# Performance work log

Measured on AMD Instinct MI355X. Metric: run time of the kernel, lower is better.

The kernel has to match this reference:

```python
import jax, jax.numpy as jnp
import numpy as np

DIM = 256          # channels
HEADS = 8
KS = 3             # kernel_size
DIL = (1, 2, 3, 4) # dilation rates
ND = len(DIL)
HEAD_DIM = DIM // HEADS
SCALE = HEAD_DIM ** -0.5
DPG = DIM // ND    # channels per dilation group
EPS = 1e-5


def setup_inputs() -> dict:
    key = jax.random.key(0)
    ks = jax.random.split(key, 4)
    B, H, W = 8, 64, 64
    vi = jax.random.normal(ks[0], (B, DIM, H, W), jnp.float32)
    ir = jax.random.normal(ks[1], (B, DIM, H, W), jnp.float32)
    w_qkv = jax.random.normal(ks[2], (3 * DIM, DIM), jnp.float32) * 0.02  # 1x1 conv, no bias (qkv_bias=False)
    proj_w = jax.random.normal(ks[3], (DIM, DIM), jnp.float32) * 0.02     # nn.Linear weight
    proj_b = jnp.zeros((DIM,), jnp.float32)
    ln_g = jnp.ones((DIM,), jnp.float32)
    ln_b = jnp.zeros((DIM,), jnp.float32)
    return dict(vi=vi, ir=ir, w_qkv=w_qkv, proj_w=proj_w, proj_b=proj_b, ln_g=ln_g, ln_b=ln_b)


def _unfold(t, dil):
    # t: [B, d, H, W] -> [B, d, KS*KS, H, W], same layout as nn.Unfold(KS, dil, pad=dil*(KS-1)//2)
    B, d, H, W = t.shape
    pad = dil * (KS - 1) // 2
    tp = jnp.pad(t, ((0, 0), (0, 0), (pad, pad), (pad, pad)))
    patches = [tp[:, :, i * dil:i * dil + H, j * dil:j * dil + W]
               for i in range(KS) for j in range(KS)]
    return jnp.stack(patches, axis=2)


def _dilate_attention(q, k, v, dil):
    # q,k,v: [B, d, H, W] with d = DPG; returns [B, H, W, d]
    B, d, H, W = q.shape
    h = d // HEAD_DIM
    N = H * W
    kk = KS * KS
    qf = q.reshape(B, h, HEAD_DIM, N)                      # b h d n
    kf = _unfold(k, dil).reshape(B, h, HEAD_DIM, kk, N)    # b h d k n
    vf = _unfold(v, dil).reshape(B, h, HEAD_DIM, kk, N)
    attn = jax.nn.softmax(jnp.einsum('bhdn,bhdkn->bhnk', qf, kf) * SCALE, axis=-1)
    out = jnp.einsum('bhnk,bhdkn->bhnd', attn, vf)         # b h n d
    return out.transpose(0, 2, 1, 3).reshape(B, H, W, d)   # channel = head*HEAD_DIM + c


def _dilate_block(x, w_qkv, proj_w, proj_b, ln_g, ln_b):
    # x: [B, C, H, W]; DilateBlock: permute -> LN -> MultiDilatelocalAttention -> residual -> permute back
    B, C, H, W = x.shape
    xn = x.transpose(0, 2, 3, 1)                           # B H W C
    mu = jnp.mean(xn, -1, keepdims=True)
    var = jnp.var(xn, -1, keepdims=True)
    xn = (xn - mu) * jax.lax.rsqrt(var + EPS) * ln_g + ln_b
    xc = xn.transpose(0, 3, 1, 2)                          # B C H W
    # 1x1 conv qkv -> [B, 3, ND, DPG, H, W]
    qkv = jnp.einsum('oc,bchw->bohw', w_qkv, xc).reshape(B, 3, ND, DPG, H, W)
    outs = [_dilate_attention(qkv[:, 0, i], qkv[:, 1, i], qkv[:, 2, i], DIL[i])
            for i in range(ND)]                            # each [B, H, W, DPG]
    y = jnp.stack(outs, axis=3).reshape(B, H, W, C)        # channel = dil_idx*DPG + c
    y = y @ proj_w.T + proj_b                              # nn.Linear
    return x + y.transpose(0, 3, 1, 2)                     # residual, back to B C H W


def reference(vi, ir, w_qkv, proj_w, proj_b, ln_g, ln_b):
    sub = vi - ir
    div = _dilate_block(sub, w_qkv, proj_w, proj_b, ln_g, ln_b)
    o = jnp.matmul(vi, div)   # batched [H,W]@[H,W] over (B, C)
    return (o, o)
```

## Files before the change

### kernel.cpp

```cpp
#include <hip/hip_runtime.h>
#include <math.h>

#define B_ 8
#define C_ 256
#define N_ 4096
#define NPOS 32768
#define SCALE_ 0.1767766952966369f
#define EPS_ 1e-5f

typedef __attribute__((ext_vector_type(8))) short bf16x8;
typedef __attribute__((ext_vector_type(8))) unsigned short u16x8;
typedef __attribute__((ext_vector_type(4))) unsigned short u16x4;
typedef __attribute__((ext_vector_type(4))) float f32x4;

__device__ __forceinline__ unsigned short f2bf(float f) {
  union { float f; unsigned u; } v; v.f = f;
  unsigned r = v.u + 0x7fff + ((v.u >> 16) & 1);
  return (unsigned short)(r >> 16);
}
__device__ __forceinline__ float bf2f(unsigned short u) {
  union { unsigned u; float f; } v; v.u = ((unsigned)u) << 16; return v.f;
}
__device__ __forceinline__ float blo(unsigned u) {
  union { unsigned u; float f; } v; v.u = u << 16; return v.f;
}
__device__ __forceinline__ float bhi(unsigned u) {
  union { unsigned u; float f; } v; v.u = u & 0xffff0000u; return v.f;
}

#define GLD_LDS16(g, l) \
  __builtin_amdgcn_global_load_lds((const __attribute__((address_space(1))) unsigned int*)(g), \
                                   (__attribute__((address_space(3))) unsigned int*)(l), 16, 0, 0)

__global__ __launch_bounds__(256) void k_cvt(
    const float* __restrict__ wq, const float* __restrict__ pw,
    unsigned short* __restrict__ dst)
{
  int i4 = blockIdx.x * 256 + threadIdx.x;
  float4 v = (i4 < 49152) ? ((const float4*)wq)[i4] : ((const float4*)pw)[i4 - 49152];
  ushort4 o;
  o.x = f2bf(v.x); o.y = f2bf(v.y); o.z = f2bf(v.z); o.w = f2bf(v.w);
  ((ushort4*)dst)[i4] = o;
}

__global__ __launch_bounds__(256) void k_sub_ln(
    const float* __restrict__ vi, const float* __restrict__ ir,
    const float* __restrict__ ln_g, const float* __restrict__ ln_b,
    unsigned short* __restrict__ subB, unsigned short* __restrict__ xn)
{
  __shared__ float tile[C_ * 33];
  __shared__ float redS[8][32], redS2[8][32];
  __shared__ float meanS[32], rstdS[32];
  int blk = blockIdx.x;
  int b = blk >> 7;
  int y = (blk >> 1) & 63;
  int half = blk & 1;
  int t = threadIdx.x;
  size_t base = (size_t)b * C_ * N_ + (size_t)y * 64 + half * 32;
  #pragma unroll
  for (int it = 0; it < 8; ++it) {
    int c = it * 32 + (t >> 3);
    int xq = (t & 7) * 4;
    size_t g = base + (size_t)c * N_ + xq;
    float4 v4 = *(const float4*)&vi[g];
    float4 i4 = *(const float4*)&ir[g];
    float4 s4;
    s4.x = v4.x - i4.x; s4.y = v4.y - i4.y; s4.z = v4.z - i4.z; s4.w = v4.w - i4.w;
    ushort4 sb;
    sb.x = f2bf(s4.x); sb.y = f2bf(s4.y); sb.z = f2bf(s4.z); sb.w = f2bf(s4.w);
    *(ushort4*)&subB[g] = sb;
    tile[c * 33 + xq + 0] = s4.x;
    tile[c * 33 + xq + 1] = s4.y;
    tile[c * 33 + xq + 2] = s4.z;
    tile[c * 33 + xq + 3] = s4.w;
  }
  __syncthreads();
  {
    int p = t & 31, grp = t >> 5;
    float s = 0.f, s2 = 0.f;
    #pragma unroll
    for (int cc = 0; cc < 32; ++cc) {
      float v = tile[(grp * 32 + cc) * 33 + p];
      s += v; s2 += v * v;
    }
    redS[grp][p] = s; redS2[grp][p] = s2;
  }
  __syncthreads();
  if (t < 32) {
    float s = 0.f, s2 = 0.f;
    #pragma unroll
    for (int g2 = 0; g2 < 8; ++g2) { s += redS[g2][t]; s2 += redS2[g2][t]; }
    float mu = s * (1.f / 256.f);
    float var = s2 * (1.f / 256.f) - mu * mu;
    meanS[t] = mu;
    rstdS[t] = rsqrtf(var + EPS_);
  }
  __syncthreads();
  int c = t;
  float gg = ln_g[c], bb = ln_b[c];
  size_t xbase = ((size_t)b * N_ + (size_t)y * 64 + half * 32) * C_;
  for (int p = 0; p < 32; ++p) {
    float v = (tile[c * 33 + p] - meanS[p]) * rstdS[p] * gg + bb;
    xn[xbase + (size_t)p * C_ + c] = f2bf(v);
  }
}

template<int EPI>
__global__ __launch_bounds__(256) void k_gemm_mfma(
    const unsigned short* __restrict__ A,
    const unsigned short* __restrict__ Bw,
    unsigned short* __restrict__ Cout,
    const float* __restrict__ bias,
    const unsigned short* __restrict__ subB,
    int ldc)
{
  __shared__ __align__(16) unsigned short As[128 * 32];
  __shared__ __align__(16) unsigned short Bs[128 * 32];
  __shared__ __align__(16) unsigned short Cs[64 * 136];
  int tid = threadIdx.x;
  int wv = tid >> 6;
  int lane = tid & 63;
  int m0 = blockIdx.x * 128;
  int n0 = blockIdx.y * 128;
  int mw = (wv >> 1) * 64, nw = (wv & 1) * 64;
  int r = lane & 15, q = lane >> 4;

  int seg0 = wv * 2;
  int srow0 = seg0 * 16 + (lane >> 2);
  int scol = (lane & 3) * 8;
  const unsigned short* ga0 = A  + (size_t)(m0 + srow0) * 256 + scol;
  const unsigned short* ga1 = ga0 + 16 * 256;
  const unsigned short* gb0 = Bw + (size_t)(n0 + srow0) * 256 + scol;
  const unsigned short* gb1 = gb0 + 16 * 256;
  unsigned short* la0 = &As[seg0 * 512];
  unsigned short* la1 = la0 + 512;
  unsigned short* lb0 = &Bs[seg0 * 512];
  unsigned short* lb1 = lb0 + 512;

  f32x4 acc[4][4];
  #pragma unroll
  for (int i = 0; i < 4; ++i)
    #pragma unroll
    for (int j = 0; j < 4; ++j)
      acc[i][j] = (f32x4){0.f, 0.f, 0.f, 0.f};

  for (int k0 = 0; k0 < 256; k0 += 32) {
    GLD_LDS16(ga0 + k0, la0);
    GLD_LDS16(ga1 + k0, la1);
    GLD_LDS16(gb0 + k0, lb0);
    GLD_LDS16(gb1 + k0, lb1);
    __syncthreads();
    bf16x8 af[4], bfr[4];
    #pragma unroll
    for (int mt = 0; mt < 4; ++mt)
      af[mt] = *(const bf16x8*)&As[(mw + mt * 16 + r) * 32 + q * 8];
    #pragma unroll
    for (int nt = 0; nt < 4; ++nt)
      bfr[nt] = *(const bf16x8*)&Bs[(nw + nt * 16 + r) * 32 + q * 8];
    #pragma unroll
    for (int mt = 0; mt < 4; ++mt)
      #pragma unroll
      for (int nt = 0; nt < 4; ++nt)
        acc[mt][nt] = __builtin_amdgcn_mfma_f32_16x16x32_bf16(af[mt], bfr[nt], acc[mt][nt], 0, 0, 0);
    __syncthreads();
  }

  int b = m0 >> 12;
  int nn0 = m0 & 4095;
  #pragma unroll
  for (int pass = 0; pass < 2; ++pass) {
    __syncthreads();
    if (EPI == 0) {
      if ((wv >> 1) == pass) {
        #pragma unroll
        for (int mt = 0; mt < 4; ++mt) {
          int lr = mt * 16 + q * 4;
          #pragma unroll
          for (int nt = 0; nt < 4; ++nt) {
            int col = nw + nt * 16 + r;
            #pragma unroll
            for (int rr = 0; rr < 4; ++rr)
              Cs[(lr + rr) * 136 + col] = f2bf(acc[mt][nt][rr]);
          }
        }
      }
    } else {
      if ((wv & 1) == pass) {
        #pragma unroll
        for (int nt = 0; nt < 4; ++nt) {
          int lr = nt * 16 + r;
          #pragma unroll
          for (int mt = 0; mt < 4; ++mt) {
            int pc = mw + mt * 16 + q * 4;
            #pragma unroll
            for (int rr = 0; rr < 4; ++rr)
              Cs[lr * 136 + pc + rr] = f2bf(acc[mt][nt][rr]);
          }
        }
      }
    }
    __syncthreads();
    if (EPI == 0) {
      #pragma unroll
      for (int cc = 0; cc < 4; ++cc) {
        int ch = cc * 256 + tid;
        int row = ch >> 4, cg = ch & 15;
        u16x8 cv = *(const u16x8*)&Cs[row * 136 + cg * 8];
        int m = m0 + pass * 64 + row;
        *(u16x8*)&Cout[(size_t)m * ldc + n0 + cg * 8] = cv;
      }
    } else {
      #pragma unroll
      for (int cc = 0; cc < 4; ++cc) {
        int ch = cc * 256 + tid;
        int row = ch >> 4, cg = ch & 15;
        u16x8 cv = *(const u16x8*)&Cs[row * 136 + cg * 8];
        int c = n0 + pass * 64 + row;
        size_t idx = ((size_t)(b * 256 + c)) * 4096 + nn0 + cg * 8;
        u16x8 sv = *(const u16x8*)&subB[idx];
        float bb = bias[c];
        u16x8 ov;
        #pragma unroll
        for (int e = 0; e < 8; ++e)
          ov[e] = f2bf(bf2f((unsigned short)cv[e]) + bb + bf2f((unsigned short)sv[e]));
        *(u16x8*)&Cout[idx] = ov;
      }
    }
  }
}

__global__ __launch_bounds__(256) void k_attn(
    const unsigned short* __restrict__ qkv,
    unsigned short* __restrict__ y)
{
  int t = threadIdx.x;
  int sub = t >> 2;
  int lane4 = t & 3;
  int item = blockIdx.x * 64 + sub;
  int ih = item & 7;
  int p = item >> 3;
  int i = ih >> 1, h = ih & 1;
  int dil = i + 1;
  int b = p >> 12;
  int n = p & 4095;
  int py = n >> 6, px = n & 63;
  int off = i * 64 + h * 32 + lane4 * 8;
  const unsigned short* base = qkv + off;

  uint4 qw = *(const uint4*)(base + (size_t)p * 768);
  float q0 = blo(qw.x), q1 = bhi(qw.x), q2 = blo(qw.y), q3 = bhi(qw.y),
        q4 = blo(qw.z), q5 = bhi(qw.z), q6 = blo(qw.w), q7 = bhi(qw.w);

  int pj[9];
  #pragma unroll
  for (int j = 0; j < 9; ++j) {
    int ny = py + (j / 3 - 1) * dil;
    int nx = px + (j % 3 - 1) * dil;
    bool ok = ((unsigned)ny < 64u) && ((unsigned)nx < 64u);
    pj[j] = ok ? ((b << 12) + (ny << 6) + nx) : -1;
  }

  float sc[9];
  #pragma unroll
  for (int j = 0; j < 9; ++j) {
    float s = 0.f;
    if (pj[j] >= 0) {
      uint4 kw = *(const uint4*)(base + 256 + (size_t)pj[j] * 768);
      s  = q0 * blo(kw.x) + q1 * bhi(kw.x);
      s += q2 * blo(kw.y) + q3 * bhi(kw.y);
      s += q4 * blo(kw.z) + q5 * bhi(kw.z);
      s += q6 * blo(kw.w) + q7 * bhi(kw.w);
    }
    s += __shfl_xor(s, 1, 4);
    s += __shfl_xor(s, 2, 4);
    sc[j] = s * SCALE_;
  }

  float mx = sc[0];
  #pragma unroll
  for (int j = 1; j < 9; ++j) mx = fmaxf(mx, sc[j]);
  float e[9], ssum = 0.f;
  #pragma unroll
  for (int j = 0; j < 9; ++j) { e[j] = __expf(sc[j] - mx); ssum += e[j]; }
  float inv = 1.f / ssum;

  float o0 = 0.f, o1 = 0.f, o2 = 0.f, o3 = 0.f, o4 = 0.f, o5 = 0.f, o6 = 0.f, o7 = 0.f;
  #pragma unroll
  for (int j = 0; j < 9; ++j) {
    if (pj[j] >= 0) {
      float w = e[j] * inv;
      uint4 vw = *(const uint4*)(base + 512 + (size_t)pj[j] * 768);
      o0 += w * blo(vw.x); o1 += w * bhi(vw.x);
      o2 += w * blo(vw.y); o3 += w * bhi(vw.y);
      o4 += w * blo(vw.z); o5 += w * bhi(vw.z);
      o6 += w * blo(vw.w); o7 += w * bhi(vw.w);
    }
  }

  u16x8 ov;
  ov[0] = f2bf(o0); ov[1] = f2bf(o1); ov[2] = f2bf(o2); ov[3] = f2bf(o3);
  ov[4] = f2bf(o4); ov[5] = f2bf(o5); ov[6] = f2bf(o6); ov[7] = f2bf(o7);
  *(u16x8*)(y + (size_t)p * 256 + off) = ov;
}

__global__ __launch_bounds__(256) void k_bmm(
    const float* __restrict__ vi, const unsigned short* __restrict__ divmB,
    float* __restrict__ out)
{
  __shared__ float At[64 * 68];
  __shared__ float Bsm[64 * 64];
  int bc = blockIdx.x;
  size_t base = (size_t)bc * 4096;
  int t = threadIdx.x;
  #pragma unroll
  for (int it = 0; it < 4; ++it) {
    int flat = it * 1024 + t * 4;
    int row = flat >> 6, col = flat & 63;
    float4 a = *(const float4*)&vi[base + flat];
    At[(col + 0) * 68 + row] = a.x;
    At[(col + 1) * 68 + row] = a.y;
    At[(col + 2) * 68 + row] = a.z;
    At[(col + 3) * 68 + row] = a.w;
  }
  #pragma unroll
  for (int it = 0; it < 2; ++it) {
    int flat = it * 2048 + t * 8;
    u16x8 dv = *(const u16x8*)&divmB[base + flat];
    float4 lo, hi;
    lo.x = bf2f((unsigned short)dv[0]); lo.y = bf2f((unsigned short)dv[1]);
    lo.z = bf2f((unsigned short)dv[2]); lo.w = bf2f((unsigned short)dv[3]);
    hi.x = bf2f((unsigned short)dv[4]); hi.y = bf2f((unsigned short)dv[5]);
    hi.z = bf2f((unsigned short)dv[6]); hi.w = bf2f((unsigned short)dv[7]);
    *(float4*)&Bsm[flat] = lo;
    *(float4*)&Bsm[flat + 4] = hi;
  }
  __syncthreads();
  int tx = t & 15, ty = t >> 4;
  float acc[4][4] = {};
  for (int k = 0; k < 64; ++k) {
    float4 a = *(const float4*)&At[k * 68 + (ty << 2)];
    float4 b = *(const float4*)&Bsm[k * 64 + (tx << 2)];
    acc[0][0] += a.x * b.x; acc[0][1] += a.x * b.y; acc[0][2] += a.x * b.z; acc[0][3] += a.x * b.w;
    acc[1][0] += a.y * b.x; acc[1][1] += a.y * b.y; acc[1][2] += a.y * b.z; acc[1][3] += a.y * b.w;
    acc[2][0] += a.z * b.x; acc[2][1] += a.z * b.y; acc[2][2] += a.z * b.z; acc[2][3] += a.z * b.w;
    acc[3][0] += a.w * b.x; acc[3][1] += a.w * b.y; acc[3][2] += a.w * b.z; acc[3][3] += a.w * b.w;
  }
  #pragma unroll
  for (int i = 0; i < 4; ++i) {
    int row = (ty << 2) + i;
    float4 w = make_float4(acc[i][0], acc[i][1], acc[i][2], acc[i][3]);
    *(float4*)&out[base + row * 64 + (tx << 2)] = w;
    *(float4*)&out[8388608ull + base + row * 64 + (tx << 2)] = w;
  }
}

extern "C" void kernel_launch(void* const* d_in, const int* in_sizes, int n_in,
                              void* d_out, int out_size, void* d_ws, size_t ws_size,
                              hipStream_t stream) {
  const float* vi     = (const float*)d_in[0];
  const float* ir     = (const float*)d_in[1];
  const float* w_qkv  = (const float*)d_in[2];
  const float* proj_w = (const float*)d_in[3];
  const float* proj_b = (const float*)d_in[4];
  const float* ln_g   = (const float*)d_in[5];
  const float* ln_b   = (const float*)d_in[6];
  float* out = (float*)d_out;
  char* ws = (char*)d_ws;
  unsigned short* subB = (unsigned short*)(ws);
  unsigned short* qkvb = (unsigned short*)(ws + 16777216);
  unsigned short* divmB= (unsigned short*)(ws + 16777216);
  unsigned short* xnb  = (unsigned short*)(ws + 67108864);
  unsigned short* yb   = (unsigned short*)(ws + 83886080);
  unsigned short* wqb  = (unsigned short*)(ws + 100663296);
  unsigned short* pwb  = wqb + 196608;

  k_cvt<<<256, 256, 0, stream>>>(w_qkv, proj_w, wqb);
  k_sub_ln<<<1024, 256, 0, stream>>>(vi, ir, ln_g, ln_b, subB, xnb);
  k_gemm_mfma<0><<<dim3(256, 6), 256, 0, stream>>>(xnb, wqb, qkvb, nullptr, nullptr, 768);
  k_attn<<<4096, 256, 0, stream>>>(qkvb, yb);
  k_gemm_mfma<1><<<dim3(256, 2), 256, 0, stream>>>(yb, pwb, divmB, proj_b, subB, 0);
  k_bmm<<<2048, 256, 0, stream>>>(vi, divmB, out);
}
```

Measured before the change: 215.4 us.

## Use bf16 MFMA for final batched matmul, fuse prep kernels, XCD-aware GEMM tiling

The final per-channel 64x64 matmul moves from fp32 FMA on LDS tiles to bf16 MFMA. It reads a bf16 copy of vi that the fused sub/LayerNorm prep kernel now writes, and the weight-conversion kernel is folded into that same launch. Both GEMMs switch to a 1D grid remapped so that consecutive M-tiles land on the same XCD, which should improve L2 locality. The cost is lower precision in the final matmul, since vi is rounded to bf16, plus an extra 16 MB write of viB and scalar output stores.

```diff
diff --git a/kernel.cpp b/kernel.cpp
--- a/kernel.cpp
+++ b/kernel.cpp
@@ -10,7 +10,6 @@
 
 typedef __attribute__((ext_vector_type(8))) short bf16x8;
 typedef __attribute__((ext_vector_type(8))) unsigned short u16x8;
-typedef __attribute__((ext_vector_type(4))) unsigned short u16x4;
 typedef __attribute__((ext_vector_type(4))) float f32x4;
 
 __device__ __forceinline__ unsigned short f2bf(float f) {
@@ -32,30 +31,30 @@
   __builtin_amdgcn_global_load_lds((const __attribute__((address_space(1))) unsigned int*)(g), \
                                    (__attribute__((address_space(3))) unsigned int*)(l), 16, 0, 0)
 
-__global__ __launch_bounds__(256) void k_cvt(
+__global__ __launch_bounds__(256) void k_pre(
+    const float* __restrict__ vi, const float* __restrict__ ir,
     const float* __restrict__ wq, const float* __restrict__ pw,
-    unsigned short* __restrict__ dst)
-{
-  int i4 = blockIdx.x * 256 + threadIdx.x;
-  float4 v = (i4 < 49152) ? ((const float4*)wq)[i4] : ((const float4*)pw)[i4 - 49152];
-  ushort4 o;
-  o.x = f2bf(v.x); o.y = f2bf(v.y); o.z = f2bf(v.z); o.w = f2bf(v.w);
-  ((ushort4*)dst)[i4] = o;
-}
-
-__global__ __launch_bounds__(256) void k_sub_ln(
-    const float* __restrict__ vi, const float* __restrict__ ir,
     const float* __restrict__ ln_g, const float* __restrict__ ln_b,
-    unsigned short* __restrict__ subB, unsigned short* __restrict__ xn)
+    unsigned short* __restrict__ wdst,
+    unsigned short* __restrict__ subB, unsigned short* __restrict__ viB,
+    unsigned short* __restrict__ xn)
 {
   __shared__ float tile[C_ * 33];
   __shared__ float redS[8][32], redS2[8][32];
   __shared__ float meanS[32], rstdS[32];
-  int blk = blockIdx.x;
+  int t = threadIdx.x;
+  if (blockIdx.x < 256) {
+    int i4 = blockIdx.x * 256 + t;
+    float4 v = (i4 < 49152) ? ((const float4*)wq)[i4] : ((const float4*)pw)[i4 - 49152];
+    ushort4 o;
+    o.x = f2bf(v.x); o.y = f2bf(v.y); o.z = f2bf(v.z); o.w = f2bf(v.w);
+    ((ushort4*)wdst)[i4] = o;
+    return;
+  }
+  int blk = blockIdx.x - 256;
   int b = blk >> 7;
   int y = (blk >> 1) & 63;
   int half = blk & 1;
-  int t = threadIdx.x;
   size_t base = (size_t)b * C_ * N_ + (size_t)y * 64 + half * 32;
   #pragma unroll
   for (int it = 0; it < 8; ++it) {
@@ -66,9 +65,11 @@
     float4 i4 = *(const float4*)&ir[g];
     float4 s4;
     s4.x = v4.x - i4.x; s4.y = v4.y - i4.y; s4.z = v4.z - i4.z; s4.w = v4.w - i4.w;
-    ushort4 sb;
+    ushort4 sb, vb;
     sb.x = f2bf(s4.x); sb.y = f2bf(s4.y); sb.z = f2bf(s4.z); sb.w = f2bf(s4.w);
+    vb.x = f2bf(v4.x); vb.y = f2bf(v4.y); vb.z = f2bf(v4.z); vb.w = f2bf(v4.w);
     *(ushort4*)&subB[g] = sb;
+    *(ushort4*)&viB[g] = vb;
     tile[c * 33 + xq + 0] = s4.x;
     tile[c * 33 + xq + 1] = s4.y;
     tile[c * 33 + xq + 2] = s4.z;
@@ -105,7 +106,7 @@
   }
 }
 
-template<int EPI>
+template<int EPI, int NT>
 __global__ __launch_bounds__(256) void k_gemm_mfma(
     const unsigned short* __restrict__ A,
     const unsigned short* __restrict__ Bw,
@@ -117,11 +118,16 @@
   __shared__ __align__(16) unsigned short As[128 * 32];
   __shared__ __align__(16) unsigned short Bs[128 * 32];
   __shared__ __align__(16) unsigned short Cs[64 * 136];
+  int flat = blockIdx.x;
+  int xcd = flat & 7;
+  int l = flat >> 3;
+  int ml = l / NT;
+  int nn = l - ml * NT;
+  int m0 = (xcd * 32 + ml) * 128;
+  int n0 = nn * 128;
   int tid = threadIdx.x;
   int wv = tid >> 6;
   int lane = tid & 63;
-  int m0 = blockIdx.x * 128;
-  int n0 = blockIdx.y * 128;
   int mw = (wv >> 1) * 64, nw = (wv & 1) * 64;
   int r = lane & 15, q = lane >> 4;
 
@@ -304,54 +310,67 @@
 }
 
 __global__ __launch_bounds__(256) void k_bmm(
-    const float* __restrict__ vi, const unsigned short* __restrict__ divmB,
+    const unsigned short* __restrict__ viB,
+    const unsigned short* __restrict__ divmB,
     float* __restrict__ out)
 {
-  __shared__ float At[64 * 68];
-  __shared__ float Bsm[64 * 64];
+  __shared__ __align__(16) unsigned short Vs[64 * 72];
+  __shared__ __align__(16) unsigned short Ds[64 * 72];
   int bc = blockIdx.x;
   size_t base = (size_t)bc * 4096;
   int t = threadIdx.x;
-  #pragma unroll
-  for (int it = 0; it < 4; ++it) {
-    int flat = it * 1024 + t * 4;
+  {
+    int flat = t * 16;
     int row = flat >> 6, col = flat & 63;
-    float4 a = *(const float4*)&vi[base + flat];
-    At[(col + 0) * 68 + row] = a.x;
-    At[(col + 1) * 68 + row] = a.y;
-    At[(col + 2) * 68 + row] = a.z;
-    At[(col + 3) * 68 + row] = a.w;
-  }
-  #pragma unroll
-  for (int it = 0; it < 2; ++it) {
-    int flat = it * 2048 + t * 8;
-    u16x8 dv = *(const u16x8*)&divmB[base + flat];
-    float4 lo, hi;
-    lo.x = bf2f((unsigned short)dv[0]); lo.y = bf2f((unsigned short)dv[1]);
-    lo.z = bf2f((unsigned short)dv[2]); lo.w = bf2f((unsigned short)dv[3]);
-    hi.x = bf2f((unsigned short)dv[4]); hi.y = bf2f((unsigned short)dv[5]);
-    hi.z = bf2f((unsigned short)dv[6]); hi.w = bf2f((unsigned short)dv[7]);
-    *(float4*)&Bsm[flat] = lo;
-    *(float4*)&Bsm[flat + 4] = hi;
+    u16x8 v0 = *(const u16x8*)&viB[base + flat];
+    u16x8 v1 = *(const u16x8*)&viB[base + flat + 8];
+    *(u16x8*)&Vs[row * 72 + col] = v0;
+    *(u16x8*)&Vs[row * 72 + col + 8] = v1;
+    u16x8 d0 = *(const u16x8*)&divmB[base + flat];
+    u16x8 d1 = *(const u16x8*)&divmB[base + flat + 8];
+    #pragma unroll
+    for (int e = 0; e < 8; ++e) {
+      Ds[(col + e) * 72 + row] = (unsigned short)d0[e];
+      Ds[(col + 8 + e) * 72 + row] = (unsigned short)d1[e];
+    }
   }
   __syncthreads();
-  int tx = t & 15, ty = t >> 4;
-  float acc[4][4] = {};
-  for (int k = 0; k < 64; ++k) {
-    float4 a = *(const float4*)&At[k * 68 + (ty << 2)];
-    float4 b = *(const float4*)&Bsm[k * 64 + (tx << 2)];
-    acc[0][0] += a.x * b.x; acc[0][1] += a.x * b.y; acc[0][2] += a.x * b.z; acc[0][3] += a.x * b.w;
-    acc[1][0] += a.y * b.x; acc[1][1] += a.y * b.y; acc[1][2] += a.y * b.z; acc[1][3] += a.y * b.w;
-    acc[2][0] += a.z * b.x; acc[2][1] += a.z * b.y; acc[2][2] += a.z * b.z; acc[2][3] += a.z * b.w;
-    acc[3][0] += a.w * b.x; acc[3][1] += a.w * b.y; acc[3][2] += a.w * b.z; acc[3][3] += a.w * b.w;
-  }
-  #pragma unroll
-  for (int i = 0; i < 4; ++i) {
-    int row = (ty << 2) + i;
-    float4 w = make_float4(acc[i][0], acc[i][1], acc[i][2], acc[i][3]);
-    *(float4*)&out[base + row * 64 + (tx << 2)] = w;
-    *(float4*)&out[8388608ull + base + row * 64 + (tx << 2)] = w;
-  }
+  int w = t >> 6, lane = t & 63;
+  int r = lane & 15, q = lane >> 4;
+  int wi = (w >> 1) * 32, wj = (w & 1) * 32;
+  f32x4 acc[2][2];
+  #pragma unroll
+  for (int i = 0; i < 2; ++i)
+    #pragma unroll
+    for (int j = 0; j < 2; ++j)
+      acc[i][j] = (f32x4){0.f, 0.f, 0.f, 0.f};
+  #pragma unroll
+  for (int ks = 0; ks < 2; ++ks) {
+    bf16x8 a[2], bfr[2];
+    #pragma unroll
+    for (int ti = 0; ti < 2; ++ti)
+      a[ti] = *(const bf16x8*)&Vs[(wi + ti * 16 + r) * 72 + ks * 32 + q * 8];
+    #pragma unroll
+    for (int tj = 0; tj < 2; ++tj)
+      bfr[tj] = *(const bf16x8*)&Ds[(wj + tj * 16 + r) * 72 + ks * 32 + q * 8];
+    #pragma unroll
+    for (int ti = 0; ti < 2; ++ti)
+      #pragma unroll
+      for (int tj = 0; tj < 2; ++tj)
+        acc[ti][tj] = __builtin_amdgcn_mfma_f32_16x16x32_bf16(a[ti], bfr[tj], acc[ti][tj], 0, 0, 0);
+  }
+  #pragma unroll
+  for (int ti = 0; ti < 2; ++ti)
+    #pragma unroll
+    for (int tj = 0; tj < 2; ++tj)
+      #pragma unroll
+      for (int rr = 0; rr < 4; ++rr) {
+        int row = wi + ti * 16 + q * 4 + rr;
+        int col = wj + tj * 16 + r;
+        float v = acc[ti][tj][rr];
+        out[base + row * 64 + col] = v;
+        out[8388608ull + base + row * 64 + col] = v;
+      }
 }
 
 extern "C" void kernel_launch(void* const* d_in, const int* in_sizes, int n_in,
@@ -371,13 +390,13 @@
   unsigned short* divmB= (unsigned short*)(ws + 16777216);
   unsigned short* xnb  = (unsigned short*)(ws + 67108864);
   unsigned short* yb   = (unsigned short*)(ws + 83886080);
-  unsigned short* wqb  = (unsigned short*)(ws + 100663296);
+  unsigned short* viB  = (unsigned short*)(ws + 100663296);
+  unsigned short* wqb  = (unsigned short*)(ws + 117440512);
   unsigned short* pwb  = wqb + 196608;
 
-  k_cvt<<<256, 256, 0, stream>>>(w_qkv, proj_w, wqb);
-  k_sub_ln<<<1024, 256, 0, stream>>>(vi, ir, ln_g, ln_b, subB, xnb);
-  k_gemm_mfma<0><<<dim3(256, 6), 256, 0, stream>>>(xnb, wqb, qkvb, nullptr, nullptr, 768);
+  k_pre<<<1280, 256, 0, stream>>>(vi, ir, w_qkv, proj_w, ln_g, ln_b, wqb, subB, viB, xnb);
+  k_gemm_mfma<0, 6><<<1536, 256, 0, stream>>>(xnb, wqb, qkvb, nullptr, nullptr, 768);
   k_attn<<<4096, 256, 0, stream>>>(qkvb, yb);
-  k_gemm_mfma<1><<<dim3(256, 2), 256, 0, stream>>>(yb, pwb, divmB, proj_b, subB, 0);
-  k_bmm<<<2048, 256, 0, stream>>>(vi, divmB, out);
-}
+  k_gemm_mfma<1, 2><<<512, 256, 0, stream>>>(yb, pwb, divmB, proj_b, subB, 0);
+  k_bmm<<<2048, 256, 0, stream>>>(viB, divmB, out);
+}
```

New measurement: 211.4 us. About the same (-1.9%).
